# Kernel optimization log

Hardware: AMD Instinct MI355X
Metric: run time of the kernel (lower is better)

## Reference

```python
import jax, jax.numpy as jnp
import numpy as np

G = 250          # grid_size hardcoded in forward
CENTER = G // 2  # 125
K = 1000         # max steps of torch.linspace(r, 2, int((2-r)*500)+1) for r in (0,1)
PAD = 1          # kernel_size // 2 for kernel_size=3
PRED = 10


def rasterize(lidar):
    """Vectorized polar_to_cartesian: lidar [B,360] -> binary grid [B,1,G,G]."""
    B = lidar.shape[0]
    dtype = lidar.dtype
    angles = jnp.linspace(0.0, 2.0 * jnp.pi, 360)            # [360]
    r = lidar                                                 # [B,360]
    valid_r = (r > 0.0) & (r < 1.0)
    # steps = int((2-r)*500) + 1  (positive -> floor == trunc)
    n = jnp.floor((2.0 - r) * 500.0).astype(jnp.int32) + 1   # [B,360], in [501,1000]
    k = jnp.arange(K, dtype=jnp.int32)                        # [K]
    denom = jnp.maximum(n - 1, 1).astype(dtype)
    # torch.linspace(r, 2, n): mag_k = r + k*(2-r)/(n-1)
    mag = r[..., None] + k.astype(dtype) * (2.0 - r)[..., None] / denom[..., None]  # [B,360,K]
    step_ok = k[None, None, :] < n[..., None]
    x = mag * jnp.cos(angles)[None, :, None]
    y = mag * jnp.sin(angles)[None, :, None]
    # int(.) truncates toward zero
    xg = jnp.trunc(CENTER + x * 100.0).astype(jnp.int32)
    yg = jnp.trunc(CENTER + y * 100.0).astype(jnp.int32)
    inb = (xg >= 0) & (xg < G) & (yg >= 0) & (yg < G)
    valid = valid_r[..., None] & step_ok & inb               # [B,360,K]
    idx = jnp.where(valid, yg * G + xg, G * G)               # invalid -> sentinel slot
    flat = jnp.zeros((B, G * G + 1), dtype=dtype)
    flat = flat.at[jnp.arange(B)[:, None, None], idx].max(valid.astype(dtype))
    return flat[:, : G * G].reshape(B, 1, G, G)


def conv2d(x, w, b):
    y = jax.lax.conv_general_dilated(
        x, w, window_strides=(1, 1), padding=[(PAD, PAD), (PAD, PAD)],
        dimension_numbers=("NCHW", "OIHW", "NCHW"))
    return y + b[None, :, None, None]


def linear(x, w, b):  # torch convention: w [out,in]
    return x @ w.T + b


def setup_inputs() -> dict:
    key = jax.random.key(0)
    ks = jax.random.split(key, 18)
    B = 8
    HW, HL = 64, 64  # hidden_size_wind, hidden_size_lidar
    conv_out = 32 * G * G  # 2,000,000

    def w(k, shape, fan_in):
        return jax.random.normal(k, shape, dtype=jnp.float32) / np.float32(np.sqrt(fan_in))

    return {
        "lidar": jax.random.uniform(ks[0], (B, 360), dtype=jnp.float32),
        "wind": jax.random.normal(ks[1], (B, 2), dtype=jnp.float32),
        "w_wind1": w(ks[2], (HW, 2), 2), "b_wind1": jnp.zeros((HW,), jnp.float32),
        "w_wind2": w(ks[3], (HW, HW), HW), "b_wind2": jnp.zeros((HW,), jnp.float32),
        "w_wind3": w(ks[4], (HW, HW), HW), "b_wind3": jnp.zeros((HW,), jnp.float32),
        "conv1_w": w(ks[5], (16, 1, 3, 3), 9), "conv1_b": jnp.zeros((16,), jnp.float32),
        "conv2_w": w(ks[6], (32, 16, 3, 3), 16 * 9), "conv2_b": jnp.zeros((32,), jnp.float32),
        "fc1_w": w(ks[7], (HL, conv_out + HW), conv_out + HW), "fc1_b": jnp.zeros((HL,), jnp.float32),
        "fc2_w": w(ks[8], (HL // 2, HL), HL), "fc2_b": jnp.zeros((HL // 2,), jnp.float32),
        "fc3_w": w(ks[9], (2 * PRED * PRED, HL // 2), HL // 2), "fc3_b": jnp.zeros((2 * PRED * PRED,), jnp.float32),
    }


def reference(lidar, wind, w_wind1, b_wind1, w_wind2, b_wind2, w_wind3, b_wind3,
              conv1_w, conv1_b, conv2_w, conv2_b, fc1_w, fc1_b, fc2_w, fc2_b, fc3_w, fc3_b):
    B = lidar.shape[0]
    img = rasterize(lidar)                                    # [B,1,250,250]
    wnd = jax.nn.relu(linear(wind, w_wind1, b_wind1))
    wnd = jax.nn.relu(linear(wnd, w_wind2, b_wind2))
    wnd = jax.nn.relu(linear(wnd, w_wind3, b_wind3))          # [B,64]
    h = jax.nn.relu(conv2d(img, conv1_w, conv1_b))            # [B,16,250,250]
    h = jax.nn.relu(conv2d(h, conv2_w, conv2_b))              # [B,32,250,250]
    h = h.reshape(B, -1)                                      # [B,2000000]
    x = jnp.concatenate([h, wnd], axis=1)
    x = jax.nn.relu(linear(x, fc1_w, fc1_b))
    x = jax.nn.relu(linear(x, fc2_w, fc2_b))
    x = linear(x, fc3_w, fc3_b)
    return x.reshape(B, PRED, PRED, 2)
```

## Files before the change

kernel.cpp:

```cpp
#include <hip/hip_runtime.h>

#define G 250
#define GG 62500
#define NB 8
#define HFEAT 2000000
#define W1STRIDE 2000064
#define NCH 7813
#define SPAN 8

typedef float f4v __attribute__((ext_vector_type(4)));

__global__ void k_raster(const float* __restrict__ lidar, float* __restrict__ img) {
    int idx = blockIdx.x * blockDim.x + threadIdx.x;
    if (idx >= NB * 360 * 1000) return;
    int k = idx % 1000;
    int ba = idx / 1000;
    int a = ba % 360;
    int b = ba / 360;
    float r = lidar[ba];
    if (!(r > 0.0f && r < 1.0f)) return;
    float tmr = __fsub_rn(2.0f, r);
    int n = (int)floorf(__fmul_rn(tmr, 500.0f)) + 1;
    if (k >= n) return;
    float denom = (float)(n - 1);
    const float delta = 6.2831855f / 359.0f;
    float angle = __fmul_rn((float)a, delta);
    float mag = __fadd_rn(r, __fdiv_rn(__fmul_rn((float)k, tmr), denom));
    float c = cosf(angle);
    float s = sinf(angle);
    float px = __fadd_rn(125.0f, __fmul_rn(__fmul_rn(mag, c), 100.0f));
    float py = __fadd_rn(125.0f, __fmul_rn(__fmul_rn(mag, s), 100.0f));
    int xg = (int)px;
    int yg = (int)py;
    if (xg >= 0 && xg < G && yg >= 0 && yg < G)
        img[b * GG + yg * G + xg] = 1.0f;
}

__global__ __launch_bounds__(256) void k_conv12(const float* __restrict__ img,
                                                const float* __restrict__ w1,
                                                const float* __restrict__ b1,
                                                const float* __restrict__ w2,
                                                const float* __restrict__ b2,
                                                float* __restrict__ h) {
    __shared__ float s_img[20][37];
    __shared__ float s_c1[16][18][35];
    __shared__ float s_w2[4608];
    __shared__ float s_w1[144];
    __shared__ float s_b1[16];
    int t = threadIdx.x;
    int bx = blockIdx.x, by = blockIdx.y, b = blockIdx.z;
    for (int i = t; i < 4608; i += 256) s_w2[i] = w2[i];
    if (t < 144) s_w1[t] = w1[t];
    if (t < 16) s_b1[t] = b1[t];
    int x0 = bx * 32 - 1, y0 = by * 16 - 1;
    for (int i = t; i < 20 * 36; i += 256) {
        int r = i / 36, c = i - r * 36;
        int gy = y0 - 1 + r, gx = x0 - 1 + c;
        float v = 0.0f;
        if (gy >= 0 && gy < G && gx >= 0 && gx < G) v = img[b * GG + gy * G + gx];
        s_img[r][c] = v;
    }
    __syncthreads();
    for (int i = t; i < 612; i += 256) {
        int yy = i / 34, xx = i - yy * 34;
        int gy = y0 + yy, gx = x0 + xx;
        bool inb = (gy >= 0 && gy < G && gx >= 0 && gx < G);
        float iv[9];
#pragma unroll
        for (int dy = 0; dy < 3; ++dy)
#pragma unroll
            for (int dx = 0; dx < 3; ++dx)
                iv[dy * 3 + dx] = s_img[yy + dy][xx + dx];
#pragma unroll
        for (int co = 0; co < 16; ++co) {
            float a = s_b1[co];
#pragma unroll
            for (int k = 0; k < 9; ++k) a = fmaf(iv[k], s_w1[co * 9 + k], a);
            s_c1[co][yy][xx] = inb ? fmaxf(a, 0.0f) : 0.0f;
        }
    }
    __syncthreads();
    int pg = t & 63;
    int cog = t >> 6;
    int ry = pg >> 2;
    int rx = (pg & 3) * 8;
    float acc[8][8];
#pragma unroll
    for (int i = 0; i < 8; ++i)
#pragma unroll
        for (int j = 0; j < 8; ++j) acc[i][j] = 0.0f;
    for (int ci = 0; ci < 16; ++ci) {
        float in[3][10];
#pragma unroll
        for (int dy = 0; dy < 3; ++dy)
#pragma unroll
            for (int xx = 0; xx < 10; ++xx)
                in[dy][xx] = s_c1[ci][ry + dy][rx + xx];
#pragma unroll
        for (int coi = 0; coi < 8; ++coi) {
            const float* wp = &s_w2[(cog * 8 + coi) * 144 + ci * 9];
            float w0 = wp[0], w1v = wp[1], w2v = wp[2], w3 = wp[3], w4 = wp[4],
                  w5 = wp[5], w6 = wp[6], w7 = wp[7], w8 = wp[8];
#pragma unroll
            for (int px = 0; px < 8; ++px) {
                float a = acc[coi][px];
                a = fmaf(in[0][px],     w0,  a);
                a = fmaf(in[0][px + 1], w1v, a);
                a = fmaf(in[0][px + 2], w2v, a);
                a = fmaf(in[1][px],     w3,  a);
                a = fmaf(in[1][px + 1], w4,  a);
                a = fmaf(in[1][px + 2], w5,  a);
                a = fmaf(in[2][px],     w6,  a);
                a = fmaf(in[2][px + 1], w7,  a);
                a = fmaf(in[2][px + 2], w8,  a);
                acc[coi][px] = a;
            }
        }
    }
    int y = by * 16 + ry;
    if (y < G) {
#pragma unroll
        for (int coi = 0; coi < 8; ++coi) {
            int co = cog * 8 + coi;
            float bv = b2[co];
#pragma unroll
            for (int px = 0; px < 8; ++px) {
                int x = bx * 32 + rx + px;
                if (x < G)
                    h[((size_t)(b * 32 + co)) * GG + y * G + x] =
                        fmaxf(acc[coi][px] + bv, 0.0f);
            }
        }
    }
}

__global__ __launch_bounds__(256) void k_fc1(const float* __restrict__ h,
                                             const float* __restrict__ W1,
                                             float* __restrict__ accout) {
    int t = threadIdx.x;
    int w = t >> 6;
    int l = t & 63;
    int s = blockIdx.x >> 1;
    int g = ((blockIdx.x & 1) << 2) | w;
    int cbeg = s * SPAN;
    if (cbeg >= NCH) return;
    int cend = min(cbeg + SPAN, NCH);

    const float* wrow[8];
#pragma unroll
    for (int oi = 0; oi < 8; ++oi)
        wrow[oi] = W1 + (size_t)(g * 8 + oi) * W1STRIDE;

    float acc[64];
#pragma unroll
    for (int i = 0; i < 64; ++i) acc[i] = 0.0f;

    for (int c = cbeg; c < cend; ++c) {
        int j = c * 256 + l * 4;
        if (j < HFEAT) {
            f4v wv[8];
            float4 hv[8];
#pragma unroll
            for (int oi = 0; oi < 8; ++oi)
                wv[oi] = __builtin_nontemporal_load((const f4v*)(wrow[oi] + j));
#pragma unroll
            for (int b = 0; b < 8; ++b)
                hv[b] = *(const float4*)(h + (size_t)b * HFEAT + j);
#pragma unroll
            for (int oi = 0; oi < 8; ++oi) {
#pragma unroll
                for (int b = 0; b < 8; ++b) {
                    float a = acc[oi * 8 + b];
                    a = fmaf(wv[oi][0], hv[b].x, a);
                    a = fmaf(wv[oi][1], hv[b].y, a);
                    a = fmaf(wv[oi][2], hv[b].z, a);
                    a = fmaf(wv[oi][3], hv[b].w, a);
                    acc[oi * 8 + b] = a;
                }
            }
        }
    }

    int cnt = 64;
#pragma unroll
    for (int st = 0; st < 6; ++st) {
        int half = cnt >> 1;
        bool up = (l >> st) & 1;
#pragma unroll
        for (int i = 0; i < half; ++i) {
            float send = up ? acc[i] : acc[i + half];
            float keep = up ? acc[i + half] : acc[i];
            float recv = __shfl_xor(send, 1 << st, 64);
            acc[i] = keep + recv;
        }
        cnt = half;
    }
    unsigned vi = __brev((unsigned)l) >> 26;
    atomicAdd(&accout[g * 64 + vi], acc[0]);
}

__global__ void k_final(const float* __restrict__ wind,
                        const float* __restrict__ ww1, const float* __restrict__ wb1,
                        const float* __restrict__ ww2, const float* __restrict__ wb2,
                        const float* __restrict__ ww3, const float* __restrict__ wb3,
                        const float* __restrict__ W1, const float* __restrict__ fb1,
                        const float* __restrict__ acc,
                        const float* __restrict__ w2, const float* __restrict__ b2,
                        const float* __restrict__ w3, const float* __restrict__ b3,
                        float* __restrict__ out) {
    __shared__ float s1[8][64], s2[8][64], f1[8][64], f2[8][32];
    int t = threadIdx.x;
    if (t < 64) {
        for (int b = 0; b < 8; ++b) {
            float v = wb1[t] + ww1[t * 2] * wind[b * 2] + ww1[t * 2 + 1] * wind[b * 2 + 1];
            s1[b][t] = fmaxf(v, 0.0f);
        }
    }
    __syncthreads();
    if (t < 64) {
        for (int b = 0; b < 8; ++b) {
            float v = wb2[t];
            for (int k = 0; k < 64; ++k) v = fmaf(s1[b][k], ww2[t * 64 + k], v);
            s2[b][t] = fmaxf(v, 0.0f);
        }
    }
    __syncthreads();
    if (t < 64) {
        for (int b = 0; b < 8; ++b) {
            float v = wb3[t];
            for (int k = 0; k < 64; ++k) v = fmaf(s2[b][k], ww3[t * 64 + k], v);
            s1[b][t] = fmaxf(v, 0.0f);
        }
    }
    __syncthreads();
    if (t < 64) {
        for (int b = 0; b < 8; ++b) {
            float v = fb1[t] + acc[t * 8 + b];
            const float* wrow = W1 + (size_t)t * W1STRIDE + HFEAT;
            for (int k = 0; k < 64; ++k) v = fmaf(s1[b][k], wrow[k], v);
            f1[b][t] = fmaxf(v, 0.0f);
        }
    }
    __syncthreads();
    if (t < 32) {
        for (int b = 0; b < 8; ++b) {
            float v = b2[t];
            for (int k = 0; k < 64; ++k) v = fmaf(f1[b][k], w2[t * 64 + k], v);
            f2[b][t] = fmaxf(v, 0.0f);
        }
    }
    __syncthreads();
    if (t < 200) {
        for (int b = 0; b < 8; ++b) {
            float v = b3[t];
            for (int k = 0; k < 32; ++k) v = fmaf(f2[b][k], w3[t * 32 + k], v);
            out[b * 200 + t] = v;
        }
    }
}

extern "C" void kernel_launch(void* const* d_in, const int* in_sizes, int n_in,
                              void* d_out, int out_size, void* d_ws, size_t ws_size,
                              hipStream_t stream) {
    const float* lidar = (const float*)d_in[0];
    const float* wind  = (const float*)d_in[1];
    const float* ww1 = (const float*)d_in[2];
    const float* wb1 = (const float*)d_in[3];
    const float* ww2 = (const float*)d_in[4];
    const float* wb2 = (const float*)d_in[5];
    const float* ww3 = (const float*)d_in[6];
    const float* wb3 = (const float*)d_in[7];
    const float* c1w = (const float*)d_in[8];
    const float* c1b = (const float*)d_in[9];
    const float* c2w = (const float*)d_in[10];
    const float* c2b = (const float*)d_in[11];
    const float* fw1 = (const float*)d_in[12];
    const float* fb1 = (const float*)d_in[13];
    const float* fw2 = (const float*)d_in[14];
    const float* fb2 = (const float*)d_in[15];
    const float* fw3 = (const float*)d_in[16];
    const float* fb3 = (const float*)d_in[17];
    float* out = (float*)d_out;

    float* ws  = (float*)d_ws;
    float* img = ws;
    float* h   = ws + 500000;
    float* acc = ws + 16500000;

    hipMemsetAsync(img, 0, 500000 * sizeof(float), stream);
    hipMemsetAsync(acc, 0, 512 * sizeof(float), stream);

    k_raster<<<(NB * 360 * 1000 + 255) / 256, 256, 0, stream>>>(lidar, img);
    dim3 g2(8, 16, NB);
    k_conv12<<<g2, 256, 0, stream>>>(img, c1w, c1b, c2w, c2b, h);
    int nblk = 2 * ((NCH + SPAN - 1) / SPAN);
    k_fc1<<<nblk, 256, 0, stream>>>(h, fw1, acc);
    k_final<<<1, 256, 0, stream>>>(wind, ww1, wb1, ww2, wb2, ww3, wb3,
                                   fw1, fb1, acc, fw2, fb2, fw3, fb3, out);
}
```

Baseline: 233.3 us.

## Double-buffer fc1 weight stream through LDS with async global_load_lds

The fc1 weight loads move from per-thread nontemporal register loads to direct global-to-LDS async loads, with two buffers per wave. Activations are loaded into two alternating register sets, and explicit vmcnt waits let chunk c+1 load while chunk c is consumed. The final partial chunk is split into a separate guarded tail path. The goal is to hide memory latency on the bandwidth-bound 512 MB weight stream, at the cost of 64 KB of LDS per block, which may lower occupancy, and hand-managed wait counts that have to match the actual number of outstanding loads.

```diff
diff --git a/kernel.cpp b/kernel.cpp
--- a/kernel.cpp
+++ b/kernel.cpp
@@ -7,8 +7,6 @@
 #define W1STRIDE 2000064
 #define NCH 7813
 #define SPAN 8
-
-typedef float f4v __attribute__((ext_vector_type(4)));
 
 __global__ void k_raster(const float* __restrict__ lidar, float* __restrict__ img) {
     int idx = blockIdx.x * blockDim.x + threadIdx.x;
@@ -134,9 +132,38 @@
     }
 }
 
+typedef __attribute__((address_space(3))) unsigned int lds_u32_t;
+typedef const __attribute__((address_space(1))) unsigned int gbl_u32_t;
+__device__ __forceinline__ void gload_lds16(const float* g, void* lds) {
+    __builtin_amdgcn_global_load_lds((gbl_u32_t*)(uintptr_t)g,
+                                     (lds_u32_t*)(unsigned int)(uintptr_t)lds,
+                                     16, 0, 0);
+}
+
+#define VMCNT16 do { asm volatile("s_waitcnt vmcnt(16)" ::: "memory"); \
+                     __builtin_amdgcn_sched_barrier(0); } while (0)
+#define VMCNT0  do { asm volatile("s_waitcnt vmcnt(0)" ::: "memory");  \
+                     __builtin_amdgcn_sched_barrier(0); } while (0)
+
+#define LOADH(HV, c) { int jh = (c) * 256 + l * 4;                               \
+    _Pragma("unroll") for (int b = 0; b < 8; ++b)                                \
+        HV[b] = *(const float4*)(h + (size_t)b * HFEAT + jh); }
+
+#define STAGEW(P, c) { _Pragma("unroll") for (int oi = 0; oi < 8; ++oi)          \
+        gload_lds16(wrow[oi] + (size_t)(c) * 256 + l * 4, &s_w[w][P][oi][0]); }
+
+#define CONSUME(P, HV) { _Pragma("unroll") for (int oi = 0; oi < 8; ++oi) {      \
+        float4 wv = *(const float4*)(&s_w[w][P][oi][l * 4]);                     \
+        _Pragma("unroll") for (int b = 0; b < 8; ++b) {                          \
+            float a = acc[oi * 8 + b];                                           \
+            a = fmaf(wv.x, HV[b].x, a); a = fmaf(wv.y, HV[b].y, a);              \
+            a = fmaf(wv.z, HV[b].z, a); a = fmaf(wv.w, HV[b].w, a);              \
+            acc[oi * 8 + b] = a; } } }
+
 __global__ __launch_bounds__(256) void k_fc1(const float* __restrict__ h,
                                              const float* __restrict__ W1,
                                              float* __restrict__ accout) {
+    __shared__ float s_w[4][2][8][256];
     int t = threadIdx.x;
     int w = t >> 6;
     int l = t & 63;
@@ -145,6 +172,7 @@
     int cbeg = s * SPAN;
     if (cbeg >= NCH) return;
     int cend = min(cbeg + SPAN, NCH);
+    int cfull = min(cend, NCH - 1);
 
     const float* wrow[8];
 #pragma unroll
@@ -155,26 +183,47 @@
 #pragma unroll
     for (int i = 0; i < 64; ++i) acc[i] = 0.0f;
 
-    for (int c = cbeg; c < cend; ++c) {
-        int j = c * 256 + l * 4;
-        if (j < HFEAT) {
-            f4v wv[8];
-            float4 hv[8];
-#pragma unroll
-            for (int oi = 0; oi < 8; ++oi)
-                wv[oi] = __builtin_nontemporal_load((const f4v*)(wrow[oi] + j));
-#pragma unroll
-            for (int b = 0; b < 8; ++b)
-                hv[b] = *(const float4*)(h + (size_t)b * HFEAT + j);
+    float4 hva[8], hvb[8];
+    int c = cbeg;
+    if (c < cfull) {
+        LOADH(hva, c)
+        STAGEW(0, c)
+        for (; c + 2 <= cfull; c += 2) {
+            LOADH(hvb, c + 1)
+            STAGEW(1, c + 1)
+            VMCNT16;
+            CONSUME(0, hva)
+            if (c + 2 < cfull) {
+                LOADH(hva, c + 2)
+                STAGEW(0, c + 2)
+                VMCNT16;
+            } else {
+                VMCNT0;
+            }
+            CONSUME(1, hvb)
+        }
+        if (c < cfull) {
+            VMCNT0;
+            CONSUME(0, hva)
+            ++c;
+        }
+    }
+
+    if (cend == NCH) {
+        int j = (NCH - 1) * 256 + l * 4;
+        if (j + 3 < HFEAT) {
+            float4 hvp, wvp;
 #pragma unroll
             for (int oi = 0; oi < 8; ++oi) {
+                wvp = *(const float4*)(wrow[oi] + j);
 #pragma unroll
                 for (int b = 0; b < 8; ++b) {
+                    hvp = *(const float4*)(h + (size_t)b * HFEAT + j);
                     float a = acc[oi * 8 + b];
-                    a = fmaf(wv[oi][0], hv[b].x, a);
-                    a = fmaf(wv[oi][1], hv[b].y, a);
-                    a = fmaf(wv[oi][2], hv[b].z, a);
-                    a = fmaf(wv[oi][3], hv[b].w, a);
+                    a = fmaf(wvp.x, hvp.x, a);
+                    a = fmaf(wvp.y, hvp.y, a);
+                    a = fmaf(wvp.z, hvp.z, a);
+                    a = fmaf(wvp.w, hvp.w, a);
                     acc[oi * 8 + b] = a;
                 }
             }
```

After: 258.2 us. 1.11x slower.
